# Performance work log

Measured on AMD Instinct MI355X. Metric: run time of the kernel, lower is better.

The kernel has to match this reference:

```python
import jax, jax.numpy as jnp
import numpy as np

B, N, C_IN = 32, 4096, 32
C_OUT = 64
K = 5            # poly_degree
P = 4            # pooling_size
NNZ = 65536      # N * avg_degree(16)


def setup_inputs() -> dict:
    key = jax.random.key(0)
    ks = jax.random.split(key, 6)
    x = jax.random.normal(ks[0], (B, N, C_IN), dtype=jnp.float32)
    # scale edge values so the Chebyshev recursion stays numerically bounded
    edge_val = jax.random.normal(ks[1], (NNZ,), dtype=jnp.float32) * 0.05
    weight = jax.random.normal(ks[2], (K * C_IN, C_OUT), dtype=jnp.float32) * 0.1
    bias = jax.random.normal(ks[3], (1, 1, C_OUT), dtype=jnp.float32) * 0.1
    edge_row = jax.random.randint(ks[4], (NNZ,), 0, N, dtype=jnp.int32)
    edge_col = jax.random.randint(ks[5], (NNZ,), 0, N, dtype=jnp.int32)
    return {"x": x, "edge_val": edge_val, "weight": weight, "bias": bias,
            "edge_row": edge_row, "edge_col": edge_col}


def reference(x, edge_val, weight, bias, edge_row, edge_col):
    b, n, c = x.shape
    out_f = weight.shape[1]
    k_deg = weight.shape[0] // c

    def spmm(v):  # sparse (COO) L @ v, v: [n, c*b]
        gathered = v[edge_col] * edge_val[:, None]          # [nnz, c*b]
        return jax.ops.segment_sum(gathered, edge_row, num_segments=n)

    # x0: [n, c*b]
    x0 = jnp.transpose(x, (1, 2, 0)).reshape(n, c * b)
    x_list = [x0]
    if k_deg > 1:
        x1 = spmm(x0)
        x_list.append(x1)
    for _ in range(2, k_deg):
        x2 = 2.0 * spmm(x1) - x0
        x_list.append(x2)
        x0, x1 = x1, x2

    xs = jnp.stack(x_list, axis=0)                          # [K, n, c, b] after reshape
    xs = xs.reshape(k_deg, n, c, b)
    xs = jnp.transpose(xs, (3, 1, 2, 0))                    # [b, n, c, K]
    xs = xs.reshape(b * n, c * k_deg)
    y = (xs @ weight).reshape(b, n, out_f)                  # dense GEMM

    y = jax.nn.relu(y + bias)                               # bias + ReLU

    if P > 1:  # max pool of size P over node dim
        y = y.reshape(b, n // P, P, out_f).max(axis=2)
    return y
```

## Files before the change

kernel.cpp:

```cpp
#include <hip/hip_runtime.h>

#define BATCH 32
#define NNODE 4096
#define CIN 32
#define COUT 64
#define KDEG 5
#define POOL 4
#define NNZ_E 65536
#define BC (BATCH * CIN)
#define TBF ((size_t)NNODE * BC)
#define CAP 64

typedef short s16x8 __attribute__((ext_vector_type(8)));
typedef float f32x4 __attribute__((ext_vector_type(4)));
typedef unsigned long long u64;

__device__ __forceinline__ unsigned short f2bf(float f) {
    union { float f; unsigned int u; } v; v.f = f;
    unsigned int u = v.u;
    u += 0x7fffu + ((u >> 16) & 1u);
    return (unsigned short)(u >> 16);
}
__device__ __forceinline__ float bf2f(unsigned short b) {
    union { float f; unsigned int u; } v; v.u = ((unsigned int)b) << 16;
    return v.f;
}
__device__ __forceinline__ u64 pack4(float a, float b, float c, float d) {
    return (u64)f2bf(a) | ((u64)f2bf(b) << 16) | ((u64)f2bf(c) << 32) | ((u64)f2bf(d) << 48);
}


__global__ void prep2_kernel(const float* __restrict__ x, unsigned short* __restrict__ t0,
                             const int* __restrict__ erow, const int* __restrict__ ecol,
                             const float* __restrict__ eval,
                             int* __restrict__ cnt, int2* __restrict__ es,
                             const float* __restrict__ W, unsigned short* __restrict__ WB) {
    int idx = blockIdx.x * 256 + threadIdx.x;
    int n   = idx >> 8;
    int rem = idx & 255;
    int b   = rem >> 3;
    int c4  = rem & 7;
    float4 v = ((const float4*)x)[(b * NNODE + n) * 8 + c4];
    ((u64*)t0)[idx] = pack4(v.x, v.y, v.z, v.w);

    if (idx < NNZ_E) {
        int r = erow[idx];
        int pos = atomicAdd(&cnt[r], 1);
        if (pos < CAP)
            es[(r << 6) + pos] = make_int2(ecol[idx], __float_as_int(eval[idx]));
    }

    if (idx < KDEG * COUT * CIN) {
        int c = idx & 31;
        int rest = idx >> 5;
        int o = rest & 63;
        int k = rest >> 6;
        WB[idx] = f2bf(W[(c * KDEG + k) * COUT + o]);
    }
}


__device__ __forceinline__ s16x8 spmm_row4(
        const unsigned short* in, const unsigned short* sub,
        float scale, int has_sub, const int* cnt, const int2* es,
        int r, int s, int lane) {
    int ep  = lane >> 4;
    int c16 = lane & 15;
    const s16x8* in16 = (const s16x8*)in;

    int deg = cnt[r]; deg = deg > CAP ? CAP : deg;
    int beg = r << 6, end = beg + deg;

    float acc[8] = {0.f,0.f,0.f,0.f,0.f,0.f,0.f,0.f};

    for (int base = beg + ep; base < end; base += 16) {
        float vv[4];
        s16x8 xx[4];
#pragma unroll
        for (int j = 0; j < 4; j++) {
            int idx = base + 4 * j;
            int src = idx < end ? idx : beg;
            int2 e = es[src];
            vv[j] = idx < end ? __int_as_float(e.y) : 0.f;
            xx[j] = in16[(size_t)e.x * 128 + s * 16 + c16];
        }
#pragma unroll
        for (int j = 0; j < 4; j++)
#pragma unroll
            for (int t = 0; t < 8; t++)
                acc[t] += vv[j] * bf2f((unsigned short)xx[j][t]);
    }

#pragma unroll
    for (int t = 0; t < 8; t++) {
        acc[t] += __shfl_xor(acc[t], 16);
        acc[t] += __shfl_xor(acc[t], 32);
    }

    union { u64 u[2]; s16x8 v; } res;
    res.u[0] = 0; res.u[1] = 0;
    if (ep == 0) {
        size_t oi = (size_t)r * 128 + s * 16 + c16;
        float rr[8];
        if (has_sub) {
            u64 sv0 = __builtin_nontemporal_load((const u64*)sub + 2 * oi);
            u64 sv1 = __builtin_nontemporal_load((const u64*)sub + 2 * oi + 1);
#pragma unroll
            for (int t = 0; t < 4; t++)
                rr[t] = scale * acc[t] - bf2f((unsigned short)(sv0 >> (16 * t)));
#pragma unroll
            for (int t = 0; t < 4; t++)
                rr[4 + t] = scale * acc[4 + t] - bf2f((unsigned short)(sv1 >> (16 * t)));
        } else {
#pragma unroll
            for (int t = 0; t < 8; t++) rr[t] = acc[t];
        }
        res.u[0] = pack4(rr[0], rr[1], rr[2], rr[3]);
        res.u[1] = pack4(rr[4], rr[5], rr[6], rr[7]);
    }
    return res.v;
}


__global__ __launch_bounds__(256, 8) void spmm_lvl_kernel(
        const unsigned short* __restrict__ in, const unsigned short* __restrict__ sub,
        unsigned short* __restrict__ out, float scale, int has_sub,
        const int* __restrict__ cnt, const int2* __restrict__ es) {
    int bx    = blockIdx.x;
    int slice = bx & 7;
    int rg    = bx >> 3;
    int wave  = threadIdx.x >> 6;
    int lane  = threadIdx.x & 63;
    int r     = rg * 4 + wave;

    s16x8 res = spmm_row4(in, sub, scale, has_sub, cnt, es, r, slice, lane);
    if (lane < 16)
        ((s16x8*)out)[(size_t)r * 128 + slice * 16 + lane] = res;
}


__global__ __launch_bounds__(1024, 8) void spmm4_gemm_kernel(
        const unsigned short* __restrict__ t3, const unsigned short* __restrict__ t2,
        const unsigned short* __restrict__ tbase, const int* __restrict__ cnt,
        const int2* __restrict__ es, const unsigned short* __restrict__ WB,
        const float* __restrict__ bias, float* __restrict__ out) {
    __shared__ s16x8 t4l[16][19];

    int tid  = threadIdx.x;
    int w    = tid >> 6;
    int lane = tid & 63;
    int bid  = blockIdx.x;
    int s    = bid & 7;
    int n0   = (bid >> 3) << 4;

    {
        int r = n0 + w;
        s16x8 res = spmm_row4(t3, t2, 2.0f, 1, cnt, es, r, s, lane);
        if (lane < 16)
            t4l[w][lane] = res;
    }
    __syncthreads();

    int m    = lane & 15;
    int q    = lane >> 4;
    int bsub = w & 3;
    int ot   = w >> 2;
    int b    = s * 4 + bsub;

    f32x4 acc = {0.f, 0.f, 0.f, 0.f};

    const unsigned short* abase = tbase + (size_t)(n0 + m) * BC + b * CIN + q * 8;
    const unsigned short* wbase = WB + m * 32 + q * 8 + (ot * 16) * 32;

#pragma unroll
    for (int k = 0; k < KDEG - 1; k++) {
        s16x8 a = *(const s16x8*)(abase + (size_t)k * TBF);
        s16x8 bf = *(const s16x8*)(wbase + (k * 64) * 32);
        acc = __builtin_amdgcn_mfma_f32_16x16x32_bf16(a, bf, acc, 0, 0, 0);
    }
    {
        s16x8 a = t4l[m][bsub * 4 + q];
        s16x8 bf = *(const s16x8*)(wbase + (4 * 64) * 32);
        acc = __builtin_amdgcn_mfma_f32_16x16x32_bf16(a, bf, acc, 0, 0, 0);
    }

    size_t orow = ((size_t)b * (NNODE / POOL) + (n0 >> 2) + q) * COUT;
    float bi = bias[ot * 16 + m];
    float r0 = acc[0] + bi; r0 = r0 > 0.f ? r0 : 0.f;
    float r1 = acc[1] + bi; r1 = r1 > 0.f ? r1 : 0.f;
    float r2 = acc[2] + bi; r2 = r2 > 0.f ? r2 : 0.f;
    float r3 = acc[3] + bi; r3 = r3 > 0.f ? r3 : 0.f;
    float mx = r0 > r1 ? r0 : r1;
    mx = mx > r2 ? mx : r2;
    mx = mx > r3 ? mx : r3;
    out[orow + ot * 16 + m] = mx;
}


extern "C" void kernel_launch(void* const* d_in, const int* in_sizes, int n_in,
                              void* d_out, int out_size, void* d_ws, size_t ws_size,
                              hipStream_t stream) {
    const float* x    = (const float*)d_in[0];
    const float* eval = (const float*)d_in[1];
    const float* W    = (const float*)d_in[2];
    const float* bias = (const float*)d_in[3];
    const int*   erow = (const int*)d_in[4];
    const int*   ecol = (const int*)d_in[5];
    float* out = (float*)d_out;

    char* base = (char*)d_ws;
    unsigned short* tb = (unsigned short*)base;
    unsigned short* t0 = tb;
    unsigned short* t1 = tb + 1 * TBF;
    unsigned short* t2 = tb + 2 * TBF;
    unsigned short* t3 = tb + 3 * TBF;

    size_t off = 5 * TBF * sizeof(unsigned short);
    int2* es = (int2*)(base + off);  off += (size_t)NNODE * CAP * sizeof(int2);
    int* cnt = (int*)(base + off);   off += (size_t)NNODE * sizeof(int);
    off += 32 * sizeof(int);
    off = (off + 63) & ~(size_t)63;
    unsigned short* WB = (unsigned short*)(base + off);

    hipMemsetAsync(cnt, 0, NNODE * sizeof(int), stream);

    prep2_kernel<<<TBF / 4 / 256, 256, 0, stream>>>(x, t0, erow, ecol, eval,
                                                    cnt, es, W, WB);

    spmm_lvl_kernel<<<NNODE * 2, 256, 0, stream>>>(t0, nullptr, t1, 1.0f, 0, cnt, es);
    spmm_lvl_kernel<<<NNODE * 2, 256, 0, stream>>>(t1, t0, t2, 2.0f, 1, cnt, es);
    spmm_lvl_kernel<<<NNODE * 2, 256, 0, stream>>>(t2, t1, t3, 2.0f, 1, cnt, es);

    spmm4_gemm_kernel<<<2048, 1024, 0, stream>>>(t3, t2, tb, cnt, es, WB, bias, out);
}
```

Before: 176.1 us.

## Unfuse last SpMM level from GEMM and compute all output tiles per wave

```diff
diff --git a/kernel.cpp b/kernel.cpp
--- a/kernel.cpp
+++ b/kernel.cpp
@@ -103,8 +103,8 @@
         size_t oi = (size_t)r * 128 + s * 16 + c16;
         float rr[8];
         if (has_sub) {
-            u64 sv0 = __builtin_nontemporal_load((const u64*)sub + 2 * oi);
-            u64 sv1 = __builtin_nontemporal_load((const u64*)sub + 2 * oi + 1);
+            u64 sv0 = ((const u64*)sub)[2 * oi];
+            u64 sv1 = ((const u64*)sub)[2 * oi + 1];
 #pragma unroll
             for (int t = 0; t < 4; t++)
                 rr[t] = scale * acc[t] - bf2f((unsigned short)(sv0 >> (16 * t)));
@@ -139,61 +139,46 @@
 }
 
 
-__global__ __launch_bounds__(1024, 8) void spmm4_gemm_kernel(
-        const unsigned short* __restrict__ t3, const unsigned short* __restrict__ t2,
-        const unsigned short* __restrict__ tbase, const int* __restrict__ cnt,
-        const int2* __restrict__ es, const unsigned short* __restrict__ WB,
+__global__ __launch_bounds__(256) void gemm_mfma_pool_kernel(
+        const unsigned short* __restrict__ tbase, const unsigned short* __restrict__ WB,
         const float* __restrict__ bias, float* __restrict__ out) {
-    __shared__ s16x8 t4l[16][19];
-
-    int tid  = threadIdx.x;
-    int w    = tid >> 6;
-    int lane = tid & 63;
-    int bid  = blockIdx.x;
-    int s    = bid & 7;
-    int n0   = (bid >> 3) << 4;
-
-    {
-        int r = n0 + w;
-        s16x8 res = spmm_row4(t3, t2, 2.0f, 1, cnt, es, r, s, lane);
-        if (lane < 16)
-            t4l[w][lane] = res;
-    }
-    __syncthreads();
-
+    int gtid = blockIdx.x * 256 + threadIdx.x;
+    int lane = threadIdx.x & 63;
+    int wid  = gtid >> 6;
+    int b    = wid >> 8;
+    int n0   = (wid & 255) << 4;
     int m    = lane & 15;
     int q    = lane >> 4;
-    int bsub = w & 3;
-    int ot   = w >> 2;
-    int b    = s * 4 + bsub;
-
-    f32x4 acc = {0.f, 0.f, 0.f, 0.f};
+
+    f32x4 acc[4] = {{0.f,0.f,0.f,0.f},{0.f,0.f,0.f,0.f},
+                    {0.f,0.f,0.f,0.f},{0.f,0.f,0.f,0.f}};
 
     const unsigned short* abase = tbase + (size_t)(n0 + m) * BC + b * CIN + q * 8;
-    const unsigned short* wbase = WB + m * 32 + q * 8 + (ot * 16) * 32;
-
-#pragma unroll
-    for (int k = 0; k < KDEG - 1; k++) {
+    const unsigned short* wbase = WB + m * 32 + q * 8;
+
+#pragma unroll
+    for (int k = 0; k < KDEG; k++) {
         s16x8 a = *(const s16x8*)(abase + (size_t)k * TBF);
-        s16x8 bf = *(const s16x8*)(wbase + (k * 64) * 32);
-        acc = __builtin_amdgcn_mfma_f32_16x16x32_bf16(a, bf, acc, 0, 0, 0);
-    }
-    {
-        s16x8 a = t4l[m][bsub * 4 + q];
-        s16x8 bf = *(const s16x8*)(wbase + (4 * 64) * 32);
-        acc = __builtin_amdgcn_mfma_f32_16x16x32_bf16(a, bf, acc, 0, 0, 0);
+#pragma unroll
+        for (int ot = 0; ot < 4; ot++) {
+            s16x8 bf = *(const s16x8*)(wbase + ((k * 64) + ot * 16) * 32);
+            acc[ot] = __builtin_amdgcn_mfma_f32_16x16x32_bf16(a, bf, acc[ot], 0, 0, 0);
+        }
     }
 
     size_t orow = ((size_t)b * (NNODE / POOL) + (n0 >> 2) + q) * COUT;
-    float bi = bias[ot * 16 + m];
-    float r0 = acc[0] + bi; r0 = r0 > 0.f ? r0 : 0.f;
-    float r1 = acc[1] + bi; r1 = r1 > 0.f ? r1 : 0.f;
-    float r2 = acc[2] + bi; r2 = r2 > 0.f ? r2 : 0.f;
-    float r3 = acc[3] + bi; r3 = r3 > 0.f ? r3 : 0.f;
-    float mx = r0 > r1 ? r0 : r1;
-    mx = mx > r2 ? mx : r2;
-    mx = mx > r3 ? mx : r3;
-    out[orow + ot * 16 + m] = mx;
+#pragma unroll
+    for (int ot = 0; ot < 4; ot++) {
+        float bi = bias[ot * 16 + m];
+        float r0 = acc[ot][0] + bi; r0 = r0 > 0.f ? r0 : 0.f;
+        float r1 = acc[ot][1] + bi; r1 = r1 > 0.f ? r1 : 0.f;
+        float r2 = acc[ot][2] + bi; r2 = r2 > 0.f ? r2 : 0.f;
+        float r3 = acc[ot][3] + bi; r3 = r3 > 0.f ? r3 : 0.f;
+        float mx = r0 > r1 ? r0 : r1;
+        mx = mx > r2 ? mx : r2;
+        mx = mx > r3 ? mx : r3;
+        out[orow + ot * 16 + m] = mx;
+    }
 }
 
 
@@ -214,6 +199,7 @@
     unsigned short* t1 = tb + 1 * TBF;
     unsigned short* t2 = tb + 2 * TBF;
     unsigned short* t3 = tb + 3 * TBF;
+    unsigned short* t4 = tb + 4 * TBF;
 
     size_t off = 5 * TBF * sizeof(unsigned short);
     int2* es = (int2*)(base + off);  off += (size_t)NNODE * CAP * sizeof(int2);
@@ -230,6 +216,8 @@
     spmm_lvl_kernel<<<NNODE * 2, 256, 0, stream>>>(t0, nullptr, t1, 1.0f, 0, cnt, es);
     spmm_lvl_kernel<<<NNODE * 2, 256, 0, stream>>>(t1, t0, t2, 2.0f, 1, cnt, es);
     spmm_lvl_kernel<<<NNODE * 2, 256, 0, stream>>>(t2, t1, t3, 2.0f, 1, cnt, es);
-
-    spmm4_gemm_kernel<<<2048, 1024, 0, stream>>>(t3, t2, tb, cnt, es, WB, bias, out);
-}
+    spmm_lvl_kernel<<<NNODE * 2, 256, 0, stream>>>(t3, t2, t4, 2.0f, 1, cnt, es);
+
+    gemm_mfma_pool_kernel<<<(BATCH * (NNODE / 16) * 64) / 256, 256, 0, stream>>>(
+        tb, WB, bias, out);
+}
```

New measurement: 166.3 us. 5.6% less time.

## Shrink fused SpMM+GEMM blocks to 256 threads with a new MFMA row mapping

Applied to the files above, without the earlier changes.

```diff
diff --git a/kernel.cpp b/kernel.cpp
--- a/kernel.cpp
+++ b/kernel.cpp
@@ -103,8 +103,8 @@
         size_t oi = (size_t)r * 128 + s * 16 + c16;
         float rr[8];
         if (has_sub) {
-            u64 sv0 = __builtin_nontemporal_load((const u64*)sub + 2 * oi);
-            u64 sv1 = __builtin_nontemporal_load((const u64*)sub + 2 * oi + 1);
+            u64 sv0 = ((const u64*)sub)[2 * oi];
+            u64 sv1 = ((const u64*)sub)[2 * oi + 1];
 #pragma unroll
             for (int t = 0; t < 4; t++)
                 rr[t] = scale * acc[t] - bf2f((unsigned short)(sv0 >> (16 * t)));
@@ -139,53 +139,51 @@
 }
 
 
-__global__ __launch_bounds__(1024, 8) void spmm4_gemm_kernel(
+__global__ __launch_bounds__(256, 8) void spmm4_gemm_kernel(
         const unsigned short* __restrict__ t3, const unsigned short* __restrict__ t2,
         const unsigned short* __restrict__ tbase, const int* __restrict__ cnt,
         const int2* __restrict__ es, const unsigned short* __restrict__ WB,
         const float* __restrict__ bias, float* __restrict__ out) {
-    __shared__ s16x8 t4l[16][19];
-
-    int tid  = threadIdx.x;
-    int w    = tid >> 6;
-    int lane = tid & 63;
-    int bid  = blockIdx.x;
-    int s    = bid & 7;
-    int n0   = (bid >> 3) << 4;
+    __shared__ s16x8 t4l[4][17];
+
+    int bx    = blockIdx.x;
+    int s     = bx & 7;
+    int rg    = bx >> 3;
+    int wv    = threadIdx.x >> 6;
+    int lane  = threadIdx.x & 63;
 
     {
-        int r = n0 + w;
+        int r = rg * 4 + wv;
         s16x8 res = spmm_row4(t3, t2, 2.0f, 1, cnt, es, r, s, lane);
         if (lane < 16)
-            t4l[w][lane] = res;
+            t4l[wv][lane] = res;
     }
     __syncthreads();
 
-    int m    = lane & 15;
-    int q    = lane >> 4;
-    int bsub = w & 3;
-    int ot   = w >> 2;
-    int b    = s * 4 + bsub;
+    int m  = lane & 15;
+    int q  = lane >> 4;
+    int dn = m & 3;
+    int bs = m >> 2;
+    int n  = rg * 4 + dn;
+    int b  = s * 4 + bs;
 
     f32x4 acc = {0.f, 0.f, 0.f, 0.f};
-
-    const unsigned short* abase = tbase + (size_t)(n0 + m) * BC + b * CIN + q * 8;
-    const unsigned short* wbase = WB + m * 32 + q * 8 + (ot * 16) * 32;
-
-#pragma unroll
-    for (int k = 0; k < KDEG - 1; k++) {
-        s16x8 a = *(const s16x8*)(abase + (size_t)k * TBF);
-        s16x8 bf = *(const s16x8*)(wbase + (k * 64) * 32);
+    const unsigned short* abase = tbase + (size_t)n * BC + b * CIN + q * 8;
+    const unsigned short* wbase = WB + (wv * 16 + m) * 32 + q * 8;
+
+#pragma unroll
+    for (int kc = 0; kc < 4; kc++) {
+        s16x8 a  = *(const s16x8*)(abase + (size_t)kc * TBF);
+        s16x8 bf = *(const s16x8*)(wbase + (kc * 64) * 32);
         acc = __builtin_amdgcn_mfma_f32_16x16x32_bf16(a, bf, acc, 0, 0, 0);
     }
     {
-        s16x8 a = t4l[m][bsub * 4 + q];
+        s16x8 a  = t4l[dn][bs * 4 + q];
         s16x8 bf = *(const s16x8*)(wbase + (4 * 64) * 32);
         acc = __builtin_amdgcn_mfma_f32_16x16x32_bf16(a, bf, acc, 0, 0, 0);
     }
 
-    size_t orow = ((size_t)b * (NNODE / POOL) + (n0 >> 2) + q) * COUT;
-    float bi = bias[ot * 16 + m];
+    float bi = bias[wv * 16 + m];
     float r0 = acc[0] + bi; r0 = r0 > 0.f ? r0 : 0.f;
     float r1 = acc[1] + bi; r1 = r1 > 0.f ? r1 : 0.f;
     float r2 = acc[2] + bi; r2 = r2 > 0.f ? r2 : 0.f;
@@ -193,7 +191,7 @@
     float mx = r0 > r1 ? r0 : r1;
     mx = mx > r2 ? mx : r2;
     mx = mx > r3 ? mx : r3;
-    out[orow + ot * 16 + m] = mx;
+    out[((size_t)(s * 4 + q) * (NNODE / POOL) + rg) * COUT + wv * 16 + m] = mx;
 }
 
 
@@ -231,5 +229,6 @@
     spmm_lvl_kernel<<<NNODE * 2, 256, 0, stream>>>(t1, t0, t2, 2.0f, 1, cnt, es);
     spmm_lvl_kernel<<<NNODE * 2, 256, 0, stream>>>(t2, t1, t3, 2.0f, 1, cnt, es);
 
-    spmm4_gemm_kernel<<<2048, 1024, 0, stream>>>(t3, t2, tb, cnt, es, WB, bias, out);
-}
+    spmm4_gemm_kernel<<<NNODE * 2, 256, 0, stream>>>(t3, t2, tb, cnt, es, WB,
+                                                     bias, out);
+}
```

Result: no change. 174.5 us (-0.9%).
